# Kernel optimization log

Hardware: AMD Instinct MI355X
Metric: run time of the kernel (lower is better)

Reference implementation:

```python
import jax, jax.numpy as jnp
import numpy as np

DIM = 640
HEADS = 10
HEAD_DIM = DIM // HEADS
SCALE = DIM ** (-0.5)  # note: module scales by full dim**-0.5, not head_dim


def setup_inputs() -> dict:
    key = jax.random.key(0)
    ks = jax.random.split(key, 5)
    B, N = 16, 1024
    x = jax.random.normal(ks[0], (B, N, DIM), dtype=jnp.float32)
    w_qkv = jax.random.normal(ks[1], (DIM, 3 * DIM), dtype=jnp.float32) * (DIM ** -0.5)
    b_qkv = jnp.zeros((3 * DIM,), dtype=jnp.float32)
    w_out = jax.random.normal(ks[2], (DIM, DIM), dtype=jnp.float32) * (DIM ** -0.5)
    b_out = jnp.zeros((DIM,), dtype=jnp.float32)
    return {"x": x, "w_qkv": w_qkv, "b_qkv": b_qkv, "w_out": w_out, "b_out": b_out}


def reference(x, w_qkv, b_qkv, w_out, b_out):
    B, N, _ = x.shape
    qkv = x @ w_qkv + b_qkv                     # [B, N, 3*DIM]
    qkv = qkv.reshape(B, N, 3, HEADS, HEAD_DIM)
    q, k, v = qkv[:, :, 0], qkv[:, :, 1], qkv[:, :, 2]   # [B, N, H, Dh]
    # scores: QK^T scaled by dim**-0.5 (module's normfactor)
    scores = jnp.einsum('bihd,bjhd->bhij', q, k) * SCALE  # [B, H, N, N]
    attn = jax.nn.softmax(scores, axis=-1)
    out = jnp.einsum('bhij,bjhd->bihd', attn, v)          # [B, N, H, Dh]
    out = out.reshape(B, N, DIM)
    return out @ w_out + b_out
```

## Files before the change

### kernel.cpp

```cpp
#include <hip/hip_runtime.h>

#define DIM 640
#define NHEADS 10
#define HDIM 64
#define SEQ 1024
#define BATCH 16
#define MROWS (BATCH * SEQ)
#define QKVN (3 * DIM)
#define NBH (BATCH * NHEADS)

typedef float f32x4 __attribute__((ext_vector_type(4)));
typedef __bf16 bf16x8 __attribute__((ext_vector_type(8)));

#define SM_C 0.057027536f

__device__ __forceinline__ unsigned short f2b(float f) {
  union { __bf16 h; unsigned short u; } v;
  v.h = (__bf16)f;
  return v.u;
}

__device__ __forceinline__ f32x4 mfma16(bf16x8 a, bf16x8 b, f32x4 c) {
  return __builtin_amdgcn_mfma_f32_16x16x32_bf16(a, b, c, 0, 0, 0);
}

typedef __attribute__((address_space(3))) unsigned int as3_u32;
typedef const __attribute__((address_space(1))) unsigned int as1_u32;
__device__ __forceinline__ void glds16(const unsigned short* g, unsigned short* l) {
  __builtin_amdgcn_global_load_lds((as1_u32*)g, (as3_u32*)l, 16, 0, 0);
}

__device__ __forceinline__ int kv_remap(int y) {
  return 32 * (y >> 5) + 8 * ((y & 15) >> 2) + (y & 3) + 4 * ((y >> 4) & 1);
}

__global__ __launch_bounds__(256) void convert_x(
    const float* __restrict__ X, unsigned short* __restrict__ xb) {
  int i = (blockIdx.x * 256 + threadIdx.x) * 4;
  float4 v = *(const float4*)(X + i);
  ushort4 s;
  s.x = f2b(v.x); s.y = f2b(v.y); s.z = f2b(v.z); s.w = f2b(v.w);
  *(ushort4*)(xb + i) = s;
}

__global__ __launch_bounds__(256) void transpose_w(
    const float* __restrict__ W, unsigned short* __restrict__ Wt, int R, int C) {
  __shared__ int tile[32][33];
  const int tx = threadIdx.x & 31, ty = threadIdx.x >> 5;
  const int c0 = blockIdx.x * 32, r0 = blockIdx.y * 32;
#pragma unroll
  for (int i = 0; i < 4; ++i)
    tile[ty + 8 * i][tx] = f2b(W[(r0 + ty + 8 * i) * C + c0 + tx]);
  __syncthreads();
#pragma unroll
  for (int i = 0; i < 4; ++i)
    Wt[(c0 + ty + 8 * i) * R + r0 + tx] = (unsigned short)tile[tx][ty + 8 * i];
}

__global__ __launch_bounds__(256) void qkv_gemm(
    const unsigned short* __restrict__ A, const unsigned short* __restrict__ Bt,
    const float* __restrict__ bias,
    unsigned short* __restrict__ qw, unsigned short* __restrict__ kw,
    unsigned short* __restrict__ vtw) {
  __shared__ __attribute__((aligned(16))) unsigned short As[128 * 64];
  __shared__ __attribute__((aligned(16))) unsigned short Bs[128 * 64];
  const int t = threadIdx.x;
  const int lane = t & 63, w = t >> 6;
  const int quad = lane >> 4, cl = lane & 15;
  const int nxb = gridDim.x;
  const int flatb = blockIdx.y * nxb + blockIdx.x;
  const int cpx = (nxb * gridDim.y) >> 3;
  const int swz = (flatb & 7) * cpx + (flatb >> 3);
  const int m0 = (swz / nxb) * 128, n0 = (swz % nxb) * 128;
  const int wr = (w >> 1) * 64, wc = (w & 1) * 64;

  const int r8 = lane >> 3;
  const int sw = ((lane & 7) ^ r8) * 8;
  const unsigned short* asrc = A + (size_t)(m0 + w * 32 + r8) * DIM + sw;
  const unsigned short* bsrc = Bt + (size_t)(n0 + w * 32 + r8) * DIM + sw;

  const int x = cl & 7;
  const int aoff0 = (wr + cl) * 64 + (quad ^ x) * 8;
  const int aoff1 = (wr + cl) * 64 + ((4 + quad) ^ x) * 8;
  const int boff0 = (wc + cl) * 64 + (quad ^ x) * 8;
  const int boff1 = (wc + cl) * 64 + ((4 + quad) ^ x) * 8;

  f32x4 acc[4][4];
#pragma unroll
  for (int i = 0; i < 4; ++i)
#pragma unroll
    for (int j = 0; j < 4; ++j) acc[i][j] = (f32x4){0.f, 0.f, 0.f, 0.f};

  for (int kt = 0; kt < DIM / 64; ++kt) {
    __syncthreads();
#pragma unroll
    for (int i = 0; i < 4; ++i) {
      glds16(asrc + (size_t)i * 8 * DIM, &As[(w * 32 + i * 8) * 64]);
      glds16(bsrc + (size_t)i * 8 * DIM, &Bs[(w * 32 + i * 8) * 64]);
    }
    asrc += 64; bsrc += 64;
    __syncthreads();
#pragma unroll
    for (int ks = 0; ks < 2; ++ks) {
      const int ao = ks ? aoff1 : aoff0, bo = ks ? boff1 : boff0;
      bf16x8 af[4], bfr[4];
#pragma unroll
      for (int i = 0; i < 4; ++i) af[i] = *(const bf16x8*)&As[ao + i * 1024];
#pragma unroll
      for (int j = 0; j < 4; ++j) bfr[j] = *(const bf16x8*)&Bs[bo + j * 1024];
#pragma unroll
      for (int i = 0; i < 4; ++i)
#pragma unroll
        for (int j = 0; j < 4; ++j) acc[i][j] = mfma16(af[i], bfr[j], acc[i][j]);
    }
  }

  const int sec = n0 / DIM;
  unsigned short* qk = (sec == 0) ? qw : kw;
  const float sc = (sec == 0) ? SM_C : 1.0f;
#pragma unroll
  for (int j = 0; j < 4; ++j) {
    int cc = n0 + wc + j * 16 + cl;
    int cr = cc - sec * DIM;
    int h = cr >> 6, d = cr & 63;
    float bv = bias[cc];
#pragma unroll
    for (int i = 0; i < 4; ++i) {
      int rbase = m0 + wr + i * 16 + quad * 4;
      int b = rbase >> 10, n = rbase & 1023;
      int bh = b * NHEADS + h;
      if (sec < 2) {
        size_t base = ((size_t)bh * SEQ + n) * HDIM + d;
#pragma unroll
        for (int r = 0; r < 4; ++r)
          qk[base + (size_t)r * HDIM] = f2b((acc[i][j][r] + bv) * sc);
      } else {
        ushort4 s;
        s.x = f2b(acc[i][j][0] + bv);
        s.y = f2b(acc[i][j][1] + bv);
        s.z = f2b(acc[i][j][2] + bv);
        s.w = f2b(acc[i][j][3] + bv);
        *(ushort4*)(vtw + ((size_t)bh * HDIM + d) * SEQ + n) = s;
      }
    }
  }
}

__global__ __launch_bounds__(256) void attn_kernel(
    const unsigned short* __restrict__ qw, const unsigned short* __restrict__ kw,
    const unsigned short* __restrict__ vtw, unsigned short* __restrict__ out) {
  __shared__ __attribute__((aligned(16))) unsigned short Ks[3][64 * 64];
  __shared__ __attribute__((aligned(16))) unsigned short Vs[3][64 * 64];
  const int t = threadIdx.x;
  const int lane = t & 63, w = t >> 6;
  const int quad = lane >> 4, cl = lane & 15;
  const int flat = blockIdx.x;
  const int bh = flat % NBH;
  const int qb = flat / NBH;
  const size_t qkbase = (size_t)bh * SEQ * HDIM;
  const size_t vbase  = (size_t)bh * HDIM * SEQ;

  const int r8 = lane >> 3;
  const int sw = ((lane & 7) ^ r8) * 8;
  const int y0 = w * 16 + r8;
  const int y1 = w * 16 + 8 + r8;
  const unsigned short* ksrc0 = kw + qkbase + (size_t)kv_remap(y0) * HDIM + sw;
  const unsigned short* ksrc1 = kw + qkbase + (size_t)kv_remap(y1) * HDIM + sw;
  const unsigned short* vsrc  = vtw + vbase + (size_t)(w * 16 + r8) * SEQ + sw;

  const int x = cl & 7;
  const int koff0 = cl * 64 + (quad ^ x) * 8;
  const int koff1 = cl * 64 + ((4 + quad) ^ x) * 8;

  bf16x8 aq[2][2];
#pragma unroll
  for (int i = 0; i < 2; ++i) {
    const unsigned short* qp =
        qw + qkbase + (size_t)(qb * 128 + w * 32 + i * 16 + cl) * HDIM;
    aq[i][0] = *(const bf16x8*)(qp + quad * 8);
    aq[i][1] = *(const bf16x8*)(qp + 32 + quad * 8);
  }

  union { unsigned short u[8]; bf16x8 v; } ow;
#pragma unroll
  for (int j = 0; j < 8; ++j) ow.u[j] = 0x3F80;
  const bf16x8 ones8 = ow.v;

  f32x4 o_acc[2][4];
#pragma unroll
  for (int i = 0; i < 2; ++i)
#pragma unroll
    for (int dt = 0; dt < 4; ++dt) o_acc[i][dt] = (f32x4){0.f, 0.f, 0.f, 0.f};
  f32x4 o1[2];
  o1[0] = (f32x4){0.f, 0.f, 0.f, 0.f};
  o1[1] = (f32x4){0.f, 0.f, 0.f, 0.f};

  auto stageKV = [&](int b, int tile) {
    const unsigned short* kp0 = ksrc0 + (size_t)tile * 64 * HDIM;
    const unsigned short* kp1 = ksrc1 + (size_t)tile * 64 * HDIM;
    const unsigned short* vp  = vsrc + tile * 64;
    glds16(kp0,          &Ks[b][(w * 16) * 64]);
    glds16(kp1,          &Ks[b][(w * 16 + 8) * 64]);
    glds16(vp,           &Vs[b][(w * 16) * 64]);
    glds16(vp + 8 * SEQ, &Vs[b][(w * 16 + 8) * 64]);
  };

  stageKV(0, 0);
  stageKV(1, 1);

  for (int kt = 0; kt < 16; ++kt) {
    if (kt < 15) asm volatile("s_waitcnt vmcnt(4)" ::: "memory");
    else         asm volatile("s_waitcnt vmcnt(0)" ::: "memory");
    __builtin_amdgcn_s_barrier();

    if (kt + 2 < 16) stageKV((kt + 2) % 3, kt + 2);

    const int cur = kt % 3;
    const unsigned short* Kc = &Ks[cur][0];
    const unsigned short* Vc = &Vs[cur][0];

    __builtin_amdgcn_s_setprio(1);

    bf16x8 pfr[2][2];
#pragma unroll
    for (int c = 0; c < 2; ++c) {
      bf16x8 ka0 = *(const bf16x8*)&Kc[koff0 + c * 2048];
      bf16x8 ka1 = *(const bf16x8*)&Kc[koff1 + c * 2048];
      bf16x8 kb0 = *(const bf16x8*)&Kc[koff0 + c * 2048 + 1024];
      bf16x8 kb1 = *(const bf16x8*)&Kc[koff1 + c * 2048 + 1024];
#pragma unroll
      for (int i = 0; i < 2; ++i) {
        f32x4 zA = (f32x4){0.f, 0.f, 0.f, 0.f};
        zA = mfma16(ka0, aq[i][0], zA);
        zA = mfma16(ka1, aq[i][1], zA);
        f32x4 zB = (f32x4){0.f, 0.f, 0.f, 0.f};
        zB = mfma16(kb0, aq[i][0], zB);
        zB = mfma16(kb1, aq[i][1], zB);
        union { unsigned short u[8]; bf16x8 v; } pk;
#pragma unroll
        for (int r = 0; r < 4; ++r) {
          pk.u[r]     = f2b(__builtin_amdgcn_exp2f(zA[r]));
          pk.u[4 + r] = f2b(__builtin_amdgcn_exp2f(zB[r]));
        }
        pfr[i][c] = pk.v;
        o1[i] = mfma16(pfr[i][c], ones8, o1[i]);
      }
    }

#pragma unroll
    for (int dt = 0; dt < 4; ++dt) {
      const int vrow = dt * 16 + cl;
      const int vx = vrow & 7;
#pragma unroll
      for (int c = 0; c < 2; ++c) {
        bf16x8 bv = *(const bf16x8*)&Vc[vrow * 64 + ((4 * c + quad) ^ vx) * 8];
#pragma unroll
        for (int i = 0; i < 2; ++i)
          o_acc[i][dt] = mfma16(pfr[i][c], bv, o_acc[i][dt]);
      }
    }

    __builtin_amdgcn_s_setprio(0);
  }

  const int b = bh / NHEADS, h = bh % NHEADS;
#pragma unroll
  for (int i = 0; i < 2; ++i)
#pragma unroll
    for (int r = 0; r < 4; ++r) {
      float inv = 1.f / o1[i][r];
      int row = b * SEQ + qb * 128 + w * 32 + i * 16 + quad * 4 + r;
#pragma unroll
      for (int dt = 0; dt < 4; ++dt)
        out[(size_t)row * DIM + h * HDIM + dt * 16 + cl] =
            f2b(o_acc[i][dt][r] * inv);
    }
}

__global__ __launch_bounds__(256) void out_gemm(
    const unsigned short* __restrict__ A, const unsigned short* __restrict__ Bt,
    const float* __restrict__ bias, float* __restrict__ C) {
  __shared__ __attribute__((aligned(16))) unsigned short As[128 * 64];
  __shared__ __attribute__((aligned(16))) unsigned short Bs[128 * 64];
  const int t = threadIdx.x;
  const int lane = t & 63, w = t >> 6;
  const int quad = lane >> 4, cl = lane & 15;
  const int nxb = gridDim.x;
  const int flatb = blockIdx.y * nxb + blockIdx.x;
  const int cpx = (nxb * gridDim.y) >> 3;
  const int swz = (flatb & 7) * cpx + (flatb >> 3);
  const int m0 = (swz / nxb) * 128, n0 = (swz % nxb) * 128;
  const int wr = (w >> 1) * 64, wc = (w & 1) * 64;

  const int r8 = lane >> 3;
  const int sw = ((lane & 7) ^ r8) * 8;
  const unsigned short* asrc = A + (size_t)(m0 + w * 32 + r8) * DIM + sw;
  const unsigned short* bsrc = Bt + (size_t)(n0 + w * 32 + r8) * DIM + sw;

  const int x = cl & 7;
  const int aoff0 = (wr + cl) * 64 + (quad ^ x) * 8;
  const int aoff1 = (wr + cl) * 64 + ((4 + quad) ^ x) * 8;
  const int boff0 = (wc + cl) * 64 + (quad ^ x) * 8;
  const int boff1 = (wc + cl) * 64 + ((4 + quad) ^ x) * 8;

  f32x4 acc[4][4];
#pragma unroll
  for (int i = 0; i < 4; ++i)
#pragma unroll
    for (int j = 0; j < 4; ++j) acc[i][j] = (f32x4){0.f, 0.f, 0.f, 0.f};

  for (int kt = 0; kt < DIM / 64; ++kt) {
    __syncthreads();
#pragma unroll
    for (int i = 0; i < 4; ++i) {
      glds16(asrc + (size_t)i * 8 * DIM, &As[(w * 32 + i * 8) * 64]);
      glds16(bsrc + (size_t)i * 8 * DIM, &Bs[(w * 32 + i * 8) * 64]);
    }
    asrc += 64; bsrc += 64;
    __syncthreads();
#pragma unroll
    for (int ks = 0; ks < 2; ++ks) {
      const int ao = ks ? aoff1 : aoff0, bo = ks ? boff1 : boff0;
      bf16x8 af[4], bfr[4];
#pragma unroll
      for (int i = 0; i < 4; ++i) af[i] = *(const bf16x8*)&As[ao + i * 1024];
#pragma unroll
      for (int j = 0; j < 4; ++j) bfr[j] = *(const bf16x8*)&Bs[bo + j * 1024];
#pragma unroll
      for (int i = 0; i < 4; ++i)
#pragma unroll
        for (int j = 0; j < 4; ++j) acc[i][j] = mfma16(af[i], bfr[j], acc[i][j]);
    }
  }
#pragma unroll
  for (int j = 0; j < 4; ++j) {
    int cc = n0 + wc + j * 16 + cl;
    float bv = bias[cc];
#pragma unroll
    for (int i = 0; i < 4; ++i) {
#pragma unroll
      for (int r = 0; r < 4; ++r) {
        int rr = m0 + wr + i * 16 + quad * 4 + r;
        C[(size_t)rr * DIM + cc] = acc[i][j][r] + bv;
      }
    }
  }
}

extern "C" void kernel_launch(void* const* d_in, const int* in_sizes, int n_in,
                              void* d_out, int out_size, void* d_ws, size_t ws_size,
                              hipStream_t stream) {
  const float* x     = (const float*)d_in[0];
  const float* w_qkv = (const float*)d_in[1];
  const float* b_qkv = (const float*)d_in[2];
  const float* w_out = (const float*)d_in[3];
  const float* b_out = (const float*)d_in[4];
  float* out = (float*)d_out;

  unsigned short* ws = (unsigned short*)d_ws;
  unsigned short* xb      = ws;
  unsigned short* wt_qkv  = ws + 10485760;
  unsigned short* wt_out  = wt_qkv + 1228800;
  unsigned short* qw      = wt_out + 409600;
  unsigned short* kw      = qw + 10485760;
  unsigned short* vtw     = kw + 10485760;
  unsigned short* attn_ws = xb;

  convert_x<<<MROWS * DIM / 1024, 256, 0, stream>>>(x, xb);
  transpose_w<<<dim3(QKVN / 32, DIM / 32), 256, 0, stream>>>(w_qkv, wt_qkv, DIM, QKVN);
  transpose_w<<<dim3(DIM / 32, DIM / 32), 256, 0, stream>>>(w_out, wt_out, DIM, DIM);
  qkv_gemm<<<dim3(QKVN / 128, MROWS / 128), 256, 0, stream>>>(xb, wt_qkv, b_qkv, qw, kw, vtw);
  attn_kernel<<<dim3(NBH * (SEQ / 128)), 256, 0, stream>>>(qw, kw, vtw, attn_ws);
  out_gemm<<<dim3(DIM / 128, MROWS / 128), 256, 0, stream>>>(attn_ws, wt_out, b_out, out);
}
```

Baseline: 233.5 us.

## Triple-buffer GEMM K-tiles with async global-to-LDS prefetch

Both the QKV and output projection GEMMs now split K into 32-wide tiles held in a three-stage LDS ring. Two tiles are prefetched ahead through direct global-to-LDS loads, synchronised by vmcnt waits and a single barrier per step instead of two syncthreads. The aim is to overlap global memory latency with MFMA work. LDS usage rises from 32KB to 48KB per block, the swizzle is redone for 32-wide rows, and there are twice as many loop iterations, each with fewer MFMAs.

```diff
diff --git a/kernel.cpp b/kernel.cpp
--- a/kernel.cpp
+++ b/kernel.cpp
@@ -62,8 +62,8 @@
     const float* __restrict__ bias,
     unsigned short* __restrict__ qw, unsigned short* __restrict__ kw,
     unsigned short* __restrict__ vtw) {
-  __shared__ __attribute__((aligned(16))) unsigned short As[128 * 64];
-  __shared__ __attribute__((aligned(16))) unsigned short Bs[128 * 64];
+  __shared__ __attribute__((aligned(16))) unsigned short As[3][128 * 32];
+  __shared__ __attribute__((aligned(16))) unsigned short Bs[3][128 * 32];
   const int t = threadIdx.x;
   const int lane = t & 63, w = t >> 6;
   const int quad = lane >> 4, cl = lane & 15;
@@ -74,16 +74,15 @@
   const int m0 = (swz / nxb) * 128, n0 = (swz % nxb) * 128;
   const int wr = (w >> 1) * 64, wc = (w & 1) * 64;
 
-  const int r8 = lane >> 3;
-  const int sw = ((lane & 7) ^ r8) * 8;
-  const unsigned short* asrc = A + (size_t)(m0 + w * 32 + r8) * DIM + sw;
-  const unsigned short* bsrc = Bt + (size_t)(n0 + w * 32 + r8) * DIM + sw;
-
-  const int x = cl & 7;
-  const int aoff0 = (wr + cl) * 64 + (quad ^ x) * 8;
-  const int aoff1 = (wr + cl) * 64 + ((4 + quad) ^ x) * 8;
-  const int boff0 = (wc + cl) * 64 + (quad ^ x) * 8;
-  const int boff1 = (wc + cl) * 64 + ((4 + quad) ^ x) * 8;
+  const int srow = lane >> 2;
+  const int schunk = ((lane & 3) ^ (srow & 3)) * 8;
+  const unsigned short* asrc =
+      A + (size_t)(m0 + w * 32 + srow) * DIM + schunk;
+  const unsigned short* bsrc =
+      Bt + (size_t)(n0 + w * 32 + srow) * DIM + schunk;
+
+  const int aoff = (wr + cl) * 32 + (quad ^ (cl & 3)) * 8;
+  const int boff = (wc + cl) * 32 + (quad ^ (cl & 3)) * 8;
 
   f32x4 acc[4][4];
 #pragma unroll
@@ -91,28 +90,38 @@
 #pragma unroll
     for (int j = 0; j < 4; ++j) acc[i][j] = (f32x4){0.f, 0.f, 0.f, 0.f};
 
-  for (int kt = 0; kt < DIM / 64; ++kt) {
-    __syncthreads();
-#pragma unroll
-    for (int i = 0; i < 4; ++i) {
-      glds16(asrc + (size_t)i * 8 * DIM, &As[(w * 32 + i * 8) * 64]);
-      glds16(bsrc + (size_t)i * 8 * DIM, &Bs[(w * 32 + i * 8) * 64]);
-    }
-    asrc += 64; bsrc += 64;
-    __syncthreads();
-#pragma unroll
-    for (int ks = 0; ks < 2; ++ks) {
-      const int ao = ks ? aoff1 : aoff0, bo = ks ? boff1 : boff0;
-      bf16x8 af[4], bfr[4];
-#pragma unroll
-      for (int i = 0; i < 4; ++i) af[i] = *(const bf16x8*)&As[ao + i * 1024];
-#pragma unroll
-      for (int j = 0; j < 4; ++j) bfr[j] = *(const bf16x8*)&Bs[bo + j * 1024];
-#pragma unroll
-      for (int i = 0; i < 4; ++i)
-#pragma unroll
-        for (int j = 0; j < 4; ++j) acc[i][j] = mfma16(af[i], bfr[j], acc[i][j]);
-    }
+  auto stage = [&](int buf, int kt) {
+    const unsigned short* a_ = asrc + kt * 32;
+    const unsigned short* b_ = bsrc + kt * 32;
+#pragma unroll
+    for (int g = 0; g < 2; ++g) {
+      glds16(a_ + (size_t)g * 16 * DIM, &As[buf][(w * 32 + g * 16) * 32]);
+      glds16(b_ + (size_t)g * 16 * DIM, &Bs[buf][(w * 32 + g * 16) * 32]);
+    }
+  };
+
+  const int NT = DIM / 32;
+  stage(0, 0);
+  stage(1, 1);
+
+  for (int kt = 0; kt < NT; ++kt) {
+    if (kt < NT - 1) asm volatile("s_waitcnt vmcnt(4)" ::: "memory");
+    else             asm volatile("s_waitcnt vmcnt(0)" ::: "memory");
+    __builtin_amdgcn_s_barrier();
+
+    if (kt + 2 < NT) stage((kt + 2) % 3, kt + 2);
+
+    const unsigned short* Ap = &As[kt % 3][0];
+    const unsigned short* Bp = &Bs[kt % 3][0];
+    bf16x8 af[4], bfr[4];
+#pragma unroll
+    for (int i = 0; i < 4; ++i) af[i] = *(const bf16x8*)&Ap[aoff + i * 512];
+#pragma unroll
+    for (int j = 0; j < 4; ++j) bfr[j] = *(const bf16x8*)&Bp[boff + j * 512];
+#pragma unroll
+    for (int i = 0; i < 4; ++i)
+#pragma unroll
+      for (int j = 0; j < 4; ++j) acc[i][j] = mfma16(af[i], bfr[j], acc[i][j]);
   }
 
   const int sec = n0 / DIM;
@@ -280,8 +289,8 @@
 __global__ __launch_bounds__(256) void out_gemm(
     const unsigned short* __restrict__ A, const unsigned short* __restrict__ Bt,
     const float* __restrict__ bias, float* __restrict__ C) {
-  __shared__ __attribute__((aligned(16))) unsigned short As[128 * 64];
-  __shared__ __attribute__((aligned(16))) unsigned short Bs[128 * 64];
+  __shared__ __attribute__((aligned(16))) unsigned short As[3][128 * 32];
+  __shared__ __attribute__((aligned(16))) unsigned short Bs[3][128 * 32];
   const int t = threadIdx.x;
   const int lane = t & 63, w = t >> 6;
   const int quad = lane >> 4, cl = lane & 15;
@@ -292,16 +301,15 @@
   const int m0 = (swz / nxb) * 128, n0 = (swz % nxb) * 128;
   const int wr = (w >> 1) * 64, wc = (w & 1) * 64;
 
-  const int r8 = lane >> 3;
-  const int sw = ((lane & 7) ^ r8) * 8;
-  const unsigned short* asrc = A + (size_t)(m0 + w * 32 + r8) * DIM + sw;
-  const unsigned short* bsrc = Bt + (size_t)(n0 + w * 32 + r8) * DIM + sw;
-
-  const int x = cl & 7;
-  const int aoff0 = (wr + cl) * 64 + (quad ^ x) * 8;
-  const int aoff1 = (wr + cl) * 64 + ((4 + quad) ^ x) * 8;
-  const int boff0 = (wc + cl) * 64 + (quad ^ x) * 8;
-  const int boff1 = (wc + cl) * 64 + ((4 + quad) ^ x) * 8;
+  const int srow = lane >> 2;
+  const int schunk = ((lane & 3) ^ (srow & 3)) * 8;
+  const unsigned short* asrc =
+      A + (size_t)(m0 + w * 32 + srow) * DIM + schunk;
+  const unsigned short* bsrc =
+      Bt + (size_t)(n0 + w * 32 + srow) * DIM + schunk;
+
+  const int aoff = (wr + cl) * 32 + (quad ^ (cl & 3)) * 8;
+  const int boff = (wc + cl) * 32 + (quad ^ (cl & 3)) * 8;
 
   f32x4 acc[4][4];
 #pragma unroll
@@ -309,28 +317,38 @@
 #pragma unroll
     for (int j = 0; j < 4; ++j) acc[i][j] = (f32x4){0.f, 0.f, 0.f, 0.f};
 
-  for (int kt = 0; kt < DIM / 64; ++kt) {
-    __syncthreads();
-#pragma unroll
-    for (int i = 0; i < 4; ++i) {
-      glds16(asrc + (size_t)i * 8 * DIM, &As[(w * 32 + i * 8) * 64]);
-      glds16(bsrc + (size_t)i * 8 * DIM, &Bs[(w * 32 + i * 8) * 64]);
-    }
-    asrc += 64; bsrc += 64;
-    __syncthreads();
-#pragma unroll
-    for (int ks = 0; ks < 2; ++ks) {
-      const int ao = ks ? aoff1 : aoff0, bo = ks ? boff1 : boff0;
-      bf16x8 af[4], bfr[4];
-#pragma unroll
-      for (int i = 0; i < 4; ++i) af[i] = *(const bf16x8*)&As[ao + i * 1024];
-#pragma unroll
-      for (int j = 0; j < 4; ++j) bfr[j] = *(const bf16x8*)&Bs[bo + j * 1024];
-#pragma unroll
-      for (int i = 0; i < 4; ++i)
-#pragma unroll
-        for (int j = 0; j < 4; ++j) acc[i][j] = mfma16(af[i], bfr[j], acc[i][j]);
-    }
+  auto stage = [&](int buf, int kt) {
+    const unsigned short* a_ = asrc + kt * 32;
+    const unsigned short* b_ = bsrc + kt * 32;
+#pragma unroll
+    for (int g = 0; g < 2; ++g) {
+      glds16(a_ + (size_t)g * 16 * DIM, &As[buf][(w * 32 + g * 16) * 32]);
+      glds16(b_ + (size_t)g * 16 * DIM, &Bs[buf][(w * 32 + g * 16) * 32]);
+    }
+  };
+
+  const int NT = DIM / 32;
+  stage(0, 0);
+  stage(1, 1);
+
+  for (int kt = 0; kt < NT; ++kt) {
+    if (kt < NT - 1) asm volatile("s_waitcnt vmcnt(4)" ::: "memory");
+    else             asm volatile("s_waitcnt vmcnt(0)" ::: "memory");
+    __builtin_amdgcn_s_barrier();
+
+    if (kt + 2 < NT) stage((kt + 2) % 3, kt + 2);
+
+    const unsigned short* Ap = &As[kt % 3][0];
+    const unsigned short* Bp = &Bs[kt % 3][0];
+    bf16x8 af[4], bfr[4];
+#pragma unroll
+    for (int i = 0; i < 4; ++i) af[i] = *(const bf16x8*)&Ap[aoff + i * 512];
+#pragma unroll
+    for (int j = 0; j < 4; ++j) bfr[j] = *(const bf16x8*)&Bp[boff + j * 512];
+#pragma unroll
+    for (int i = 0; i < 4; ++i)
+#pragma unroll
+      for (int j = 0; j < 4; ++j) acc[i][j] = mfma16(af[i], bfr[j], acc[i][j]);
   }
 #pragma unroll
   for (int j = 0; j < 4; ++j) {
```

Measured after the change: 233.0 us. Within noise of the previous version (-0.2%).
